# Performance work log

Measured on AMD Instinct MI355X. Metric: run time of the kernel, lower is better.

The kernel has to match this reference:

```python
import jax, jax.numpy as jnp
import numpy as np

NUM_NODES = 9
HIDDEN = 512
BATCH = 8192
EPS = 1e-8


def _neighbor_lists(num_nodes):
    """Replicates torch.nonzero row-scan order: doubling, then complementary, then central."""
    doubling = {}
    for s, d in [(0, 1), (1, 3), (3, 7), (7, 6), (6, 4), (4, 0)]:
        if s < num_nodes and d < num_nodes:
            doubling.setdefault(d, []).append(s)
    comp = {}
    for a, b in [(0, 7), (1, 6), (3, 4), (2, 5)]:
        if a < num_nodes and b < num_nodes:
            comp.setdefault(a, []).append(b)
            comp.setdefault(b, []).append(a)
    nbrs = []
    for i in range(num_nodes):
        lst = sorted(doubling.get(i, [])) + sorted(comp.get(i, []))
        if num_nodes > 8:  # central hub node 8
            if i < 8:
                lst = lst + [8]
            elif i == 8:
                lst = lst + list(range(8))
        nbrs.append(lst)
    return nbrs


def _mobius_add(x, y, c):
    # x: (B,H) or broadcastable; Poincare-ball Mobius addition
    xy = jnp.sum(x * y, axis=-1, keepdims=True)
    xx = jnp.sum(x * x, axis=-1, keepdims=True)
    yy = jnp.sum(y * y, axis=-1, keepdims=True)
    num = (1 + 2 * c * xy + c * yy) * x + (1 - c * xx) * y
    den = 1 + 2 * c * xy + (c ** 2) * xx * yy
    return num / (den + EPS)


def setup_inputs() -> dict:
    key = jax.random.key(0)
    k0, k1, k2, k3 = jax.random.split(key, 4)
    node_features = jax.random.normal(k0, (BATCH, NUM_NODES, HIDDEN), jnp.float32)
    bound = 1.0 / np.sqrt(HIDDEN)
    to_w = jax.random.uniform(k1, (HIDDEN, HIDDEN), jnp.float32, -bound, bound)
    to_b = jnp.zeros((HIDDEN,), jnp.float32)
    from_w = jax.random.uniform(k2, (HIDDEN, HIDDEN), jnp.float32, -bound, bound)
    from_b = jnp.zeros((HIDDEN,), jnp.float32)
    # kaiming_normal with tanh gain 5/3; fan_in of (N,N,H) tensor = N*H
    std = (5.0 / 3.0) / np.sqrt(NUM_NODES * HIDDEN)
    mobius_weights = jax.random.normal(k3, (NUM_NODES, NUM_NODES, HIDDEN), jnp.float32) * std
    curvature = jnp.asarray(-1.0, jnp.float32)
    return {
        "node_features": node_features,
        "curvature": curvature,
        "to_w": to_w,
        "to_b": to_b,
        "from_w": from_w,
        "from_b": from_b,
        "mobius_weights": mobius_weights,
    }


def reference(node_features, curvature, to_w, to_b, from_w, from_b, mobius_weights):
    c = jnp.abs(curvature)
    # to_poincare_ball
    x_proj = node_features @ to_w.T + to_b                      # (B,N,H)
    norm = jnp.linalg.norm(x_proj, axis=-1, keepdims=True)
    h = jnp.tanh(norm) * x_proj / (norm + EPS)                  # (B,N,H)

    nbrs = _neighbor_lists(NUM_NODES)
    cols = []
    for i in range(NUM_NODES):  # tiny fixed structural loop (9 nodes)
        r = h[:, i]                                             # (B,H)
        for j in nbrs[i]:       # sequential (non-commutative) Mobius fold
            t = _mobius_add(h[:, j], mobius_weights[i, j][None, :], c)
            r = _mobius_add(r, t, c)
        cols.append(r)
    result = jnp.stack(cols, axis=1)                            # (B,N,H)

    # from_poincare_ball
    return result @ from_w.T + from_b
```

## Files before the change

kernel.cpp:

```cpp
#include <hip/hip_runtime.h>

typedef unsigned short u16;
typedef unsigned int u32;
typedef __bf16 bf16x8 __attribute__((ext_vector_type(8)));
typedef float floatx4 __attribute__((ext_vector_type(4)));

#define EPSF 1e-8f

__device__ __forceinline__ float bf2f(u16 u) { return __uint_as_float(((u32)u) << 16); }
__device__ __forceinline__ u16 f2bf(float f) {
  u32 u = __float_as_uint(f);
  u += 0x7fffu + ((u >> 16) & 1u);
  return (u16)(u >> 16);
}
__device__ __forceinline__ void unpack2(u32 u, float& a, float& b) {
  a = __uint_as_float(u << 16);
  b = __uint_as_float(u & 0xffff0000u);
}
__device__ __forceinline__ float wave_sum(float s) {
#pragma unroll
  for (int m = 32; m; m >>= 1) s += __shfl_xor(s, m, 64);
  return s;
}
__device__ __forceinline__ u32 cvtpk(float lo, float hi) {
  u32 r;
  asm("v_cvt_pk_bf16_f32 %0, %1, %2" : "=v"(r) : "v"(lo), "v"(hi));
  return r;
}

typedef __attribute__((address_space(1))) void gv_t;
typedef __attribute__((address_space(3))) void lv_t;
__device__ __forceinline__ void gload_lds16(const u16* g, u16* l) {
  __builtin_amdgcn_global_load_lds((const gv_t*)g, (lv_t*)l, 16, 0, 0);
}

__device__ __forceinline__ bool sniff_f32(const void* curv) {
  return ((const u16*)curv)[0] == 0;
}
__device__ __forceinline__ uint4 load8bf(const void* base, size_t off, bool isf32) {
  if (!isf32) return *(const uint4*)((const u16*)base + off);
  const float* p = (const float*)base + off;
  float4 a = *(const float4*)p;
  float4 b = *(const float4*)(p + 4);
  uint4 r;
  r.x = (u32)f2bf(a.x) | ((u32)f2bf(a.y) << 16);
  r.y = (u32)f2bf(a.z) | ((u32)f2bf(a.w) << 16);
  r.z = (u32)f2bf(b.x) | ((u32)f2bf(b.y) << 16);
  r.w = (u32)f2bf(b.z) | ((u32)f2bf(b.w) << 16);
  return r;
}
__device__ __forceinline__ void load8f(const void* base, size_t off, bool isf32, float* o) {
  if (isf32) {
    const float* p = (const float*)base + off;
    float4 a = *(const float4*)p;
    float4 b = *(const float4*)(p + 4);
    o[0] = a.x; o[1] = a.y; o[2] = a.z; o[3] = a.w;
    o[4] = b.x; o[5] = b.y; o[6] = b.z; o[7] = b.w;
  } else {
    const u16* p = (const u16*)base + off;
    uint4 r = *(const uint4*)p;
    unpack2(r.x, o[0], o[1]);
    unpack2(r.y, o[2], o[3]);
    unpack2(r.z, o[4], o[5]);
    unpack2(r.w, o[6], o[7]);
  }
}

__global__ __launch_bounds__(256) void cvt_kernel(
    const float* __restrict__ A, const float* __restrict__ TW, const float* __restrict__ FW,
    u16* __restrict__ oA, u16* __restrict__ oTW, u16* __restrict__ oFW,
    const void* __restrict__ curv)
{
  if (!sniff_f32(curv)) return;
  const long CA = 37748736L / 8;
  const long CW = 262144L / 8;
  const long total = CA + 2 * CW;
  for (long i = (long)blockIdx.x * blockDim.x + threadIdx.x; i < total;
       i += (long)gridDim.x * blockDim.x) {
    const float* s; u16* d; long j;
    if (i < CA)           { s = A;  d = oA;  j = i; }
    else if (i < CA + CW) { s = TW; d = oTW; j = i - CA; }
    else                  { s = FW; d = oFW; j = i - CA - CW; }
    float4 a = *(const float4*)(s + j * 8);
    float4 b = *(const float4*)(s + j * 8 + 4);
    uint4 o;
    o.x = cvtpk(a.x, a.y);
    o.y = cvtpk(a.z, a.w);
    o.z = cvtpk(b.x, b.y);
    o.w = cvtpk(b.z, b.w);
    *(uint4*)(d + j * 8) = o;
  }
}

template <int FINAL>
__global__ __launch_bounds__(256) void gemm_fast(
    const void* __restrict__ origA, const u16* __restrict__ convA,
    const void* __restrict__ origB, const u16* __restrict__ convB,
    const void* __restrict__ bias, void* __restrict__ out,
    const void* __restrict__ curv, int M, int N, int K)
{
  __shared__ __align__(16) u16 As[128 * 32];
  __shared__ __align__(16) u16 Bs[128 * 32];

  const bool f32 = sniff_f32(curv);
  const u16* A = f32 ? convA : (const u16*)origA;
  const u16* B = f32 ? convB : (const u16*)origB;

  const int t = threadIdx.x;
  const int lane = t & 63;
  const int w = t >> 6;
  const int waveM = w >> 1, waveN = w & 1;
  const int m0 = blockIdx.y * 128;
  const int n0 = blockIdx.x * 128;

  floatx4 acc[4][4];
#pragma unroll
  for (int i = 0; i < 4; i++)
#pragma unroll
    for (int j = 0; j < 4; j++) {
      acc[i][j][0] = 0.f; acc[i][j][1] = 0.f;
      acc[i][j][2] = 0.f; acc[i][j][3] = 0.f;
    }

  const u16* ga0 = A + (size_t)(m0 + (t >> 2)) * K + (t & 3) * 8;
  const u16* ga1 = ga0 + (size_t)64 * K;
  const u16* gb0 = B + (size_t)(n0 + (t >> 2)) * K + (t & 3) * 8;
  const u16* gb1 = gb0 + (size_t)64 * K;
  u16* lA0 = As + w * 512;
  u16* lA1 = As + 2048 + w * 512;
  u16* lB0 = Bs + w * 512;
  u16* lB1 = Bs + 2048 + w * 512;

  const int am = waveM * 64 + (lane & 15);
  const int bn = waveN * 64 + (lane & 15);
  const int kq = (lane >> 4) * 8;

  for (int k0 = 0; k0 < K; k0 += 32) {
    gload_lds16(ga0 + k0, lA0);
    gload_lds16(ga1 + k0, lA1);
    gload_lds16(gb0 + k0, lB0);
    gload_lds16(gb1 + k0, lB1);
    __syncthreads();

    bf16x8 af[4], bfr[4];
#pragma unroll
    for (int mt = 0; mt < 4; mt++)
      af[mt] = *(const bf16x8*)(As + (am + mt * 16) * 32 + kq);
#pragma unroll
    for (int nt = 0; nt < 4; nt++)
      bfr[nt] = *(const bf16x8*)(Bs + (bn + nt * 16) * 32 + kq);
#pragma unroll
    for (int mt = 0; mt < 4; mt++)
#pragma unroll
      for (int nt = 0; nt < 4; nt++)
        acc[mt][nt] = __builtin_amdgcn_mfma_f32_16x16x32_bf16(af[mt], bfr[nt], acc[mt][nt], 0, 0, 0);
    __syncthreads();
  }

  const int quad = lane >> 4;
  const int cl = lane & 15;
#pragma unroll
  for (int mt = 0; mt < 4; mt++)
#pragma unroll
    for (int nt = 0; nt < 4; nt++) {
      const int col = n0 + waveN * 64 + nt * 16 + cl;
      const float bs = f32 ? ((const float*)bias)[col] : bf2f(((const u16*)bias)[col]);
#pragma unroll
      for (int r = 0; r < 4; r++) {
        const int row = m0 + waveM * 64 + mt * 16 + quad * 4 + r;
        const float v = acc[mt][nt][r] + bs;
        if (FINAL && f32) ((float*)out)[(size_t)row * N + col] = v;
        else              ((u16*)out)[(size_t)row * N + col] = f2bf(v);
      }
    }
}

__global__ __launch_bounds__(256) void mobius2(
    u16* Xf, u16* Xb, const void* __restrict__ MW, const void* __restrict__ curv)
{
  __shared__ float h[9][512];
  __shared__ float hh[9];

  const bool f32 = sniff_f32(curv);
  u16* X = f32 ? Xf : Xb;

  const int b = blockIdx.x;
  const int t = threadIdx.x;
  const int lane = t & 63;
  const int w = t >> 6;
  const float c = f32 ? fabsf(((const float*)curv)[0]) : fabsf(bf2f(((const u16*)curv)[0]));

  for (int r = w; r < 9; r += 4) {
    uint4 raw = *(const uint4*)(X + ((size_t)b * 9 + r) * 512 + lane * 8);
    float x[8];
    unpack2(raw.x, x[0], x[1]);
    unpack2(raw.y, x[2], x[3]);
    unpack2(raw.z, x[4], x[5]);
    unpack2(raw.w, x[6], x[7]);
    float s = 0.f;
#pragma unroll
    for (int p = 0; p < 8; p++) s += x[p] * x[p];
    s = wave_sum(s);
    const float norm = sqrtf(s);
    const float scale = tanhf(norm) / (norm + EPSF);
#pragma unroll
    for (int p = 0; p < 8; p++) h[r][lane * 8 + p] = x[p] * scale;
    if (lane == 0) hh[r] = scale * scale * s;
  }
  __syncthreads();

  const int baseNode[4] = {8, 0, 3, 6};
  const int cntNode[4] = {1, 3, 3, 2};
  const int nbrCnt[9] = {3, 3, 2, 3, 3, 2, 3, 3, 8};
  const int nbrTab[9][8] = {
      {4, 7, 8, 0, 0, 0, 0, 0}, {0, 6, 8, 0, 0, 0, 0, 0}, {5, 8, 0, 0, 0, 0, 0, 0},
      {1, 4, 8, 0, 0, 0, 0, 0}, {6, 3, 8, 0, 0, 0, 0, 0}, {2, 8, 0, 0, 0, 0, 0, 0},
      {7, 1, 8, 0, 0, 0, 0, 0}, {3, 0, 8, 0, 0, 0, 0, 0}, {0, 1, 2, 3, 4, 5, 6, 7}};

  for (int s = 0; s < cntNode[w]; s++) {
    const int i = baseNode[w] + s;
    float r8[8];
#pragma unroll
    for (int p = 0; p < 8; p++) r8[p] = h[i][lane * 8 + p];
    float rr = 0.f;
#pragma unroll
    for (int p = 0; p < 8; p++) rr += r8[p] * r8[p];
    rr = wave_sum(rr);

    for (int e = 0; e < nbrCnt[i]; e++) {
      const int j = nbrTab[i][e];
      float y[8];
      load8f(MW, ((size_t)i * 9 + j) * 512 + lane * 8, f32, y);
      float x8[8];
#pragma unroll
      for (int p = 0; p < 8; p++) x8[p] = h[j][lane * 8 + p];
      const float xx = hh[j];
      float xy = 0.f, yy = 0.f;
#pragma unroll
      for (int p = 0; p < 8; p++) { xy += x8[p] * y[p]; yy += y[p] * y[p]; }
#pragma unroll
      for (int m = 32; m; m >>= 1) {
        xy += __shfl_xor(xy, m, 64);
        yy += __shfl_xor(yy, m, 64);
      }
      const float a1 = 1.f + 2.f * c * xy + c * yy;
      const float b1 = 1.f - c * xx;
      const float inv1 = 1.f / (1.f + 2.f * c * xy + c * c * xx * yy + EPSF);
      float t8[8];
#pragma unroll
      for (int p = 0; p < 8; p++) t8[p] = (a1 * x8[p] + b1 * y[p]) * inv1;
      float tt = 0.f, rt = 0.f;
#pragma unroll
      for (int p = 0; p < 8; p++) { tt += t8[p] * t8[p]; rt += r8[p] * t8[p]; }
#pragma unroll
      for (int m = 32; m; m >>= 1) {
        tt += __shfl_xor(tt, m, 64);
        rt += __shfl_xor(rt, m, 64);
      }
      const float a2 = 1.f + 2.f * c * rt + c * tt;
      const float b2 = 1.f - c * rr;
      const float inv2 = 1.f / (1.f + 2.f * c * rt + c * c * rr * tt + EPSF);
      float nrr = 0.f;
#pragma unroll
      for (int p = 0; p < 8; p++) {
        r8[p] = (a2 * r8[p] + b2 * t8[p]) * inv2;
        nrr += r8[p] * r8[p];
      }
      rr = wave_sum(nrr);
    }

    uint4 o;
    o.x = (u32)f2bf(r8[0]) | ((u32)f2bf(r8[1]) << 16);
    o.y = (u32)f2bf(r8[2]) | ((u32)f2bf(r8[3]) << 16);
    o.z = (u32)f2bf(r8[4]) | ((u32)f2bf(r8[5]) << 16);
    o.w = (u32)f2bf(r8[6]) | ((u32)f2bf(r8[7]) << 16);
    *(uint4*)(X + ((size_t)b * 9 + i) * 512 + lane * 8) = o;
  }
}

__global__ __launch_bounds__(256) void gemm1_bt_bias(
    const void* __restrict__ A, const void* __restrict__ Bw,
    const void* __restrict__ bias, void* out, void* ws,
    const void* __restrict__ curv, int M, int N, int K)
{
  __shared__ __align__(16) u16 As[128 * 32];
  __shared__ __align__(16) u16 Bs[128 * 32];

  const bool f32 = sniff_f32(curv);
  u16* C = f32 ? (u16*)ws : (u16*)out;

  const int t = threadIdx.x;
  const int lane = t & 63;
  const int w = t >> 6;
  const int waveM = w >> 1, waveN = w & 1;
  const int m0 = blockIdx.y * 128;
  const int n0 = blockIdx.x * 128;

  floatx4 acc[4][4];
#pragma unroll
  for (int i = 0; i < 4; i++)
#pragma unroll
    for (int j = 0; j < 4; j++) {
      acc[i][j][0] = 0.f; acc[i][j][1] = 0.f;
      acc[i][j][2] = 0.f; acc[i][j][3] = 0.f;
    }

  const int r0 = t >> 2;
  const int c0 = (t & 3) * 8;
  const size_t oa0 = (size_t)(m0 + r0) * K + c0;
  const size_t oa1 = (size_t)(m0 + 64 + r0) * K + c0;
  const size_t ob0 = (size_t)(n0 + r0) * K + c0;
  const size_t ob1 = (size_t)(n0 + 64 + r0) * K + c0;

  for (int k0 = 0; k0 < K; k0 += 32) {
    uint4 a0 = load8bf(A, oa0 + k0, f32);
    uint4 a1 = load8bf(A, oa1 + k0, f32);
    uint4 b0 = load8bf(Bw, ob0 + k0, f32);
    uint4 b1 = load8bf(Bw, ob1 + k0, f32);
    __syncthreads();
    *(uint4*)(As + t * 8) = a0;
    *(uint4*)(As + 2048 + t * 8) = a1;
    *(uint4*)(Bs + t * 8) = b0;
    *(uint4*)(Bs + 2048 + t * 8) = b1;
    __syncthreads();

    bf16x8 af[4], bfr[4];
    const int am = waveM * 64 + (lane & 15);
    const int bn = waveN * 64 + (lane & 15);
    const int kq = (lane >> 4) * 8;
#pragma unroll
    for (int mt = 0; mt < 4; mt++)
      af[mt] = *(const bf16x8*)(As + (am + mt * 16) * 32 + kq);
#pragma unroll
    for (int nt = 0; nt < 4; nt++)
      bfr[nt] = *(const bf16x8*)(Bs + (bn + nt * 16) * 32 + kq);
#pragma unroll
    for (int mt = 0; mt < 4; mt++)
#pragma unroll
      for (int nt = 0; nt < 4; nt++)
        acc[mt][nt] = __builtin_amdgcn_mfma_f32_16x16x32_bf16(af[mt], bfr[nt], acc[mt][nt], 0, 0, 0);
  }

  const int quad = lane >> 4;
  const int cl = lane & 15;
#pragma unroll
  for (int mt = 0; mt < 4; mt++)
#pragma unroll
    for (int nt = 0; nt < 4; nt++) {
      const int col = n0 + waveN * 64 + nt * 16 + cl;
      const float bs = f32 ? ((const float*)bias)[col] : bf2f(((const u16*)bias)[col]);
#pragma unroll
      for (int r = 0; r < 4; r++) {
        const int row = m0 + waveM * 64 + mt * 16 + quad * 4 + r;
        C[(size_t)row * N + col] = f2bf(acc[mt][nt][r] + bs);
      }
    }
}

__global__ __launch_bounds__(256) void gemm2_fullN(
    const void* __restrict__ Bw, const void* __restrict__ bias,
    void* out, void* ws, const void* __restrict__ curv,
    int M, int N, int K)
{
  __shared__ __align__(16) u16 As[32 * 32];
  __shared__ __align__(16) u16 Bs[512 * 32];

  const bool f32 = sniff_f32(curv);
  const u16* A = f32 ? (const u16*)ws : (const u16*)out;

  const int t = threadIdx.x;
  const int lane = t & 63;
  const int w = t >> 6;
  const int m0 = blockIdx.x * 32;

  floatx4 acc[2][8];
#pragma unroll
  for (int i = 0; i < 2; i++)
#pragma unroll
    for (int j = 0; j < 8; j++) {
      acc[i][j][0] = 0.f; acc[i][j][1] = 0.f;
      acc[i][j][2] = 0.f; acc[i][j][3] = 0.f;
    }

  const int r0 = t >> 2;
  const int c0 = (t & 3) * 8;

  for (int k0 = 0; k0 < K; k0 += 32) {
    uint4 av = make_uint4(0, 0, 0, 0);
    if (t < 128)
      av = *(const uint4*)(A + (size_t)(m0 + r0) * K + k0 + c0);
    uint4 bv[8];
#pragma unroll
    for (int q = 0; q < 8; q++)
      bv[q] = load8bf(Bw, (size_t)(q * 64 + r0) * K + k0 + c0, f32);
    __syncthreads();
    if (t < 128) *(uint4*)(As + t * 8) = av;
#pragma unroll
    for (int q = 0; q < 8; q++)
      *(uint4*)(Bs + q * 2048 + t * 8) = bv[q];
    __syncthreads();

    bf16x8 af[2], bfr[8];
    const int ml = lane & 15;
    const int kq = (lane >> 4) * 8;
#pragma unroll
    for (int mt = 0; mt < 2; mt++)
      af[mt] = *(const bf16x8*)(As + (mt * 16 + ml) * 32 + kq);
#pragma unroll
    for (int nt = 0; nt < 8; nt++)
      bfr[nt] = *(const bf16x8*)(Bs + (w * 128 + nt * 16 + ml) * 32 + kq);
#pragma unroll
    for (int mt = 0; mt < 2; mt++)
#pragma unroll
      for (int nt = 0; nt < 8; nt++)
        acc[mt][nt] = __builtin_amdgcn_mfma_f32_16x16x32_bf16(af[mt], bfr[nt], acc[mt][nt], 0, 0, 0);
  }

  const int quad = lane >> 4;
  const int cl = lane & 15;
#pragma unroll
  for (int mt = 0; mt < 2; mt++)
#pragma unroll
    for (int nt = 0; nt < 8; nt++) {
      const int col = w * 128 + nt * 16 + cl;
      const float bs = f32 ? ((const float*)bias)[col] : bf2f(((const u16*)bias)[col]);
#pragma unroll
      for (int r = 0; r < 4; r++) {
        const int row = m0 + mt * 16 + quad * 4 + r;
        const float v = acc[mt][nt][r] + bs;
        if (f32) ((float*)out)[(size_t)row * N + col] = v;
        else     ((u16*)out)[(size_t)row * N + col] = f2bf(v);
      }
    }
}

extern "C" void kernel_launch(void* const* d_in, const int* in_sizes, int n_in,
                              void* d_out, int out_size, void* d_ws, size_t ws_size,
                              hipStream_t stream) {
  const void* nf = d_in[0];
  const void* curv = d_in[1];
  const void* to_w = d_in[2];
  const void* to_b = d_in[3];
  const void* fr_w = d_in[4];
  const void* fr_b = d_in[5];
  const void* mw = d_in[6];

  const int M = 8192 * 9, N = 512, K = 512;
  const size_t XB = (size_t)M * N * 2;
  const size_t WWB = (size_t)512 * 512 * 2;

  u16 *xb = nullptr, *a_bf = nullptr, *tw_bf = nullptr, *fw_bf = nullptr;
  bool fast = false;
  if (ws_size >= 2 * XB + 2 * WWB) {
    xb    = (u16*)d_ws;
    a_bf  = (u16*)((char*)d_ws + XB);
    tw_bf = (u16*)((char*)d_ws + 2 * XB);
    fw_bf = (u16*)((char*)d_ws + 2 * XB + WWB);
    fast = true;
  } else if (ws_size >= XB + 2 * WWB) {
    xb    = (u16*)d_ws;
    tw_bf = (u16*)((char*)d_ws + XB);
    fw_bf = (u16*)((char*)d_ws + XB + WWB);
    a_bf  = (u16*)d_out;
    fast = true;
  } else if (ws_size >= XB + WWB) {
    xb    = (u16*)d_ws;
    fw_bf = (u16*)((char*)d_ws + XB);
    a_bf  = (u16*)d_out;
    tw_bf = (u16*)((char*)d_out + XB);
    fast = true;
  }

  if (fast) {
    cvt_kernel<<<2048, 256, 0, stream>>>((const float*)nf, (const float*)to_w,
                                         (const float*)fr_w, a_bf, tw_bf, fw_bf, curv);
    gemm_fast<0><<<dim3(N / 128, M / 128), 256, 0, stream>>>(
        nf, a_bf, to_w, tw_bf, to_b, xb, curv, M, N, K);
    mobius2<<<8192, 256, 0, stream>>>(xb, xb, mw, curv);
    gemm_fast<1><<<dim3(N / 128, M / 128), 256, 0, stream>>>(
        xb, xb, fr_w, fw_bf, fr_b, d_out, curv, M, N, K);
  } else {
    gemm1_bt_bias<<<dim3(N / 128, M / 128), 256, 0, stream>>>(nf, to_w, to_b, d_out, d_ws, curv, M, N, K);
    mobius2<<<8192, 256, 0, stream>>>((u16*)d_ws, (u16*)d_out, mw, curv);
    gemm2_fullN<<<M / 32, 256, 0, stream>>>(fr_w, fr_b, d_out, d_ws, curv, M, N, K);
  }
}
```

Measured before the change: 514.0 us.

## Derive Mobius fold norms algebraically, precompute weight norms, swizzle GEMM block order

The Mobius fold step no longer materialises t or recomputes its norms with extra wave reductions. tt, rt and the new rr are derived in closed form from xy, rx, ry and known norms. Weight squared norms are precomputed once per call by a small kernel into a device global, which cuts the per-edge reductions from four or five to three. Also adds an XCD-aware block-index swizzle to the GEMM kernel and packed bf16 conversion on store. The risk is extra rounding drift from tracking norms algebraically instead of recomputing them, plus one extra tiny kernel launch.

```diff
diff --git a/kernel.cpp b/kernel.cpp
--- a/kernel.cpp
+++ b/kernel.cpp
@@ -6,6 +6,8 @@
 typedef float floatx4 __attribute__((ext_vector_type(4)));
 
 #define EPSF 1e-8f
+
+__device__ float g_nrm[81];
 
 __device__ __forceinline__ float bf2f(u16 u) { return __uint_as_float(((u32)u) << 16); }
 __device__ __forceinline__ u16 f2bf(float f) {
@@ -64,6 +66,20 @@
     unpack2(r.z, o[4], o[5]);
     unpack2(r.w, o[6], o[7]);
   }
+}
+
+__global__ __launch_bounds__(64) void mwnorm(const void* __restrict__ MW,
+                                             const void* __restrict__ curv) {
+  const bool f32 = sniff_f32(curv);
+  const int e = blockIdx.x;
+  const int lane = threadIdx.x;
+  float y[8];
+  load8f(MW, (size_t)e * 512 + lane * 8, f32, y);
+  float s = 0.f;
+#pragma unroll
+  for (int p = 0; p < 8; p++) s += y[p] * y[p];
+  s = wave_sum(s);
+  if (lane == 0) g_nrm[e] = s;
 }
 
 __global__ __launch_bounds__(256) void cvt_kernel(
@@ -110,8 +126,12 @@
   const int lane = t & 63;
   const int w = t >> 6;
   const int waveM = w >> 1, waveN = w & 1;
-  const int m0 = blockIdx.y * 128;
-  const int n0 = blockIdx.x * 128;
+
+  int lid = blockIdx.x + blockIdx.y * gridDim.x;
+  const int nwg = gridDim.x * gridDim.y;
+  if ((nwg & 7) == 0) lid = (lid & 7) * (nwg >> 3) + (lid >> 3);
+  const int m0 = (lid / gridDim.x) * 128;
+  const int n0 = (lid % gridDim.x) * 128;
 
   floatx4 acc[4][4];
 #pragma unroll
@@ -175,7 +195,7 @@
     }
 }
 
-__global__ __launch_bounds__(256) void mobius2(
+__global__ __launch_bounds__(256) void mobius3(
     u16* Xf, u16* Xb, const void* __restrict__ MW, const void* __restrict__ curv)
 {
   __shared__ float h[9][512];
@@ -222,10 +242,7 @@
     float r8[8];
 #pragma unroll
     for (int p = 0; p < 8; p++) r8[p] = h[i][lane * 8 + p];
-    float rr = 0.f;
-#pragma unroll
-    for (int p = 0; p < 8; p++) rr += r8[p] * r8[p];
-    rr = wave_sum(rr);
+    float rr = hh[i];
 
     for (int e = 0; e < nbrCnt[i]; e++) {
       const int j = nbrTab[i][e];
@@ -234,46 +251,46 @@
       float x8[8];
 #pragma unroll
       for (int p = 0; p < 8; p++) x8[p] = h[j][lane * 8 + p];
-      const float xx = hh[j];
-      float xy = 0.f, yy = 0.f;
-#pragma unroll
-      for (int p = 0; p < 8; p++) { xy += x8[p] * y[p]; yy += y[p] * y[p]; }
+
+      float xy = 0.f, rx = 0.f, ry = 0.f;
+#pragma unroll
+      for (int p = 0; p < 8; p++) {
+        xy += x8[p] * y[p];
+        rx += r8[p] * x8[p];
+        ry += r8[p] * y[p];
+      }
 #pragma unroll
       for (int m = 32; m; m >>= 1) {
         xy += __shfl_xor(xy, m, 64);
-        yy += __shfl_xor(yy, m, 64);
+        rx += __shfl_xor(rx, m, 64);
+        ry += __shfl_xor(ry, m, 64);
       }
+
+      const float xx = hh[j];
+      const float yy = g_nrm[i * 9 + j];
       const float a1 = 1.f + 2.f * c * xy + c * yy;
       const float b1 = 1.f - c * xx;
       const float inv1 = 1.f / (1.f + 2.f * c * xy + c * c * xx * yy + EPSF);
-      float t8[8];
-#pragma unroll
-      for (int p = 0; p < 8; p++) t8[p] = (a1 * x8[p] + b1 * y[p]) * inv1;
-      float tt = 0.f, rt = 0.f;
-#pragma unroll
-      for (int p = 0; p < 8; p++) { tt += t8[p] * t8[p]; rt += r8[p] * t8[p]; }
-#pragma unroll
-      for (int m = 32; m; m >>= 1) {
-        tt += __shfl_xor(tt, m, 64);
-        rt += __shfl_xor(rt, m, 64);
-      }
+      const float tt = inv1 * inv1 * (a1 * a1 * xx + 2.f * a1 * b1 * xy + b1 * b1 * yy);
+      const float rt = inv1 * (a1 * rx + b1 * ry);
       const float a2 = 1.f + 2.f * c * rt + c * tt;
       const float b2 = 1.f - c * rr;
       const float inv2 = 1.f / (1.f + 2.f * c * rt + c * c * rr * tt + EPSF);
-      float nrr = 0.f;
-#pragma unroll
-      for (int p = 0; p < 8; p++) {
-        r8[p] = (a2 * r8[p] + b2 * t8[p]) * inv2;
-        nrr += r8[p] * r8[p];
-      }
-      rr = wave_sum(nrr);
+      const float ca = a2 * inv2;
+      const float cb = b2 * inv2 * inv1;
+      const float cx = cb * a1;
+      const float cy = cb * b1;
+#pragma unroll
+      for (int p = 0; p < 8; p++)
+        r8[p] = ca * r8[p] + cx * x8[p] + cy * y[p];
+      rr = inv2 * inv2 * (a2 * a2 * rr + 2.f * a2 * b2 * rt + b2 * b2 * tt);
     }
 
     uint4 o;
-    o.x = (u32)f2bf(r8[0]) | ((u32)f2bf(r8[1]) << 16);
-    o.y = (u32)f2bf(r8[2]) | ((u32)f2bf(r8[3]) << 16);
-    o.z = (u32)f2bf(r8[4]) | ((u32)f2bf(r8[5]) << 16);
-    o.w = (u32)f2bf(r8[6]) | ((u32)f2bf(r8[7]) << 16);
+    o.x = cvtpk(r8[0], r8[1]);
+    o.y = cvtpk(r8[2], r8[3]);
+    o.z = cvtpk(r8[4], r8[5]);
+    o.w = cvtpk(r8[6], r8[7]);
     *(uint4*)(X + ((size_t)b * 9 + i) * 512 + lane * 8) = o;
   }
 }
@@ -471,17 +488,19 @@
     fast = true;
   }
 
+  mwnorm<<<81, 64, 0, stream>>>(mw, curv);
+
   if (fast) {
     cvt_kernel<<<2048, 256, 0, stream>>>((const float*)nf, (const float*)to_w,
                                          (const float*)fr_w, a_bf, tw_bf, fw_bf, curv);
     gemm_fast<0><<<dim3(N / 128, M / 128), 256, 0, stream>>>(
         nf, a_bf, to_w, tw_bf, to_b, xb, curv, M, N, K);
-    mobius2<<<8192, 256, 0, stream>>>(xb, xb, mw, curv);
+    mobius3<<<8192, 256, 0, stream>>>(xb, xb, mw, curv);
     gemm_fast<1><<<dim3(N / 128, M / 128), 256, 0, stream>>>(
         xb, xb, fr_w, fw_bf, fr_b, d_out, curv, M, N, K);
   } else {
     gemm1_bt_bias<<<dim3(N / 128, M / 128), 256, 0, stream>>>(nf, to_w, to_b, d_out, d_ws, curv, M, N, K);
-    mobius2<<<8192, 256, 0, stream>>>((u16*)d_ws, (u16*)d_out, mw, curv);
+    mobius3<<<8192, 256, 0, stream>>>((u16*)d_ws, (u16*)d_out, mw, curv);
     gemm2_fullN<<<M / 32, 256, 0, stream>>>(fr_w, fr_b, d_out, d_ws, curv, M, N, K);
   }
 }
```

Result: faster. 474.0 us (-7.8%).
